# Kernel tuning notes

Measured on AMD Instinct MI355X. Metric: run time of the kernel, lower is better.

The kernel has to match this reference:

```python
import jax, jax.numpy as jnp
import numpy as np

N_E = 8192
E_DIM = 256
BETA = 0.25


def setup_inputs() -> dict:
    key = jax.random.key(0)
    kz, ke = jax.random.split(key)
    z = jax.random.normal(kz, (16, E_DIM, 32, 32), dtype=jnp.float32)
    embedding = jax.random.uniform(ke, (N_E, E_DIM), dtype=jnp.float32,
                                   minval=-1.0 / N_E, maxval=1.0 / N_E)
    return {"z": z, "embedding": embedding}


def reference(z, embedding):
    n_e, e_dim = embedding.shape
    # (B, C, H, W) -> (B, H, W, C) -> (N, e_dim)
    zp = jnp.transpose(z, (0, 2, 3, 1))
    zf = zp.reshape(-1, e_dim)
    # squared L2 distances: |z|^2 + |e|^2 - 2 z.e   -> (N, n_e)
    dists = (jnp.sum(zf * zf, axis=1, keepdims=True)
             + jnp.sum(embedding * embedding, axis=1)
             - 2.0 * (zf @ embedding.T))
    # two smallest distances (top-2 of negated dists)
    _, top2_idx = jax.lax.top_k(-dists, 2)
    min_encoding_indices = top2_idx[:, 0:1]
    second_encoding_indices = top2_idx[:, 1:2]
    min_encodings = jax.nn.one_hot(top2_idx[:, 0], n_e, dtype=zp.dtype)  # (N, n_e)
    z_q = (min_encodings @ embedding).reshape(zp.shape)
    # commitment / codebook loss
    loss = (jnp.mean((jax.lax.stop_gradient(z_q) - zp) ** 2)
            + BETA * jnp.mean((z_q - jax.lax.stop_gradient(zp)) ** 2))
    # straight-through estimator
    z_q = zp + jax.lax.stop_gradient(z_q - zp)
    avg_probs = jnp.mean(min_encodings, axis=0)
    perplexity = jnp.exp(-jnp.sum(avg_probs * jnp.log(avg_probs + 1e-10)))
    z_q = jnp.transpose(z_q, (0, 3, 1, 2))
    return (loss, z_q, perplexity, min_encodings,
            min_encoding_indices, second_encoding_indices)
```

## Files before the change

### kernel.cpp

```cpp
#include <hip/hip_runtime.h>
#include <cfloat>
#include <cstdint>
#include <cstddef>

#define M_ROWS 16384
#define NE     8192
#define KD     256

#define OFF_LOSS   0ULL
#define OFF_ZQ     1ULL
#define OFF_PERP   4194305ULL
#define OFF_ONEHOT 4194306ULL
#define OFF_I0     138412034ULL
#define OFF_I1     138428418ULL

#define SCR_Z16  0ULL
#define SCR_E16  2097152ULL
#define SCR_Z32T 3145728ULL
#define SCR_PART 7340032ULL

#define WS_I0    0
#define WS_HIST  16384
#define WS_ENORM 24576
#define WS_CNORM 32768
#define WS_T0SUM 49152
#define WS_TOTAL 49154

typedef _Float16 fp16x8 __attribute__((ext_vector_type(8)));
typedef float    floatx16 __attribute__((ext_vector_type(16)));

__global__ void zero_onehot_kernel(float* __restrict__ out) {
    size_t tidg = (size_t)blockIdx.x * 1024 + threadIdx.x;
    float4* base = (float4*)(out + OFF_ONEHOT + 2);
    const float4 zz = make_float4(0.f, 0.f, 0.f, 0.f);
#pragma unroll
    for (int i = 0; i < 8; i++) {
        size_t q = tidg + (size_t)i * 4194304ULL;
        if (q < 33554431ULL) base[q] = zz;
    }
    if (tidg == 0) {
        out[OFF_ONEHOT + 0] = 0.f;
        out[OFF_ONEHOT + 1] = 0.f;
        out[OFF_ONEHOT + 134217726ULL] = 0.f;
        out[OFF_ONEHOT + 134217727ULL] = 0.f;
    }
}

__global__ void scatter_ones_kernel(const int* __restrict__ ws_i0, float* __restrict__ out) {
    int r = blockIdx.x * 256 + threadIdx.x;
    int j = ws_i0[r] & (NE - 1);
    out[OFF_ONEHOT + (size_t)r * NE + j] = 1.0f;
}

__device__ __forceinline__ float pairwise16_sq(const float* row, int lane16) {
    const int h = lane16 >> 3, j = lane16 & 7;
    const float* p = row + h * 128 + j;
    float x = p[0];
    float r = __fmul_rn(x, x);
#pragma unroll
    for (int i = 1; i < 16; i++) {
        float y = p[i * 8];
        r = __fadd_rn(r, __fmul_rn(y, y));
    }
    float s = __fadd_rn(r, __shfl_xor(r, 1));
    s = __fadd_rn(s, __shfl_xor(s, 2));
    s = __fadd_rn(s, __shfl_xor(s, 4));
    s = __fadd_rn(s, __shfl_xor(s, 8));
    return s;
}

__global__ void split_e_kernel(const float* __restrict__ emb, _Float16* __restrict__ e16,
                               float* __restrict__ enorm, int* __restrict__ hist,
                               float* __restrict__ wsf) {
    __shared__ float ef[16][261];
    const int tid = threadIdx.x;
    const int row0 = blockIdx.x * 16;
#pragma unroll
    for (int p = 0; p < 4; p++) {
        int q = p * 256 + tid;
        int rl = q >> 6, kq = q & 63;
        float4 v = *(const float4*)(emb + (size_t)(row0 + rl) * KD + kq * 4);
        ef[rl][kq * 4 + 0] = v.x; ef[rl][kq * 4 + 1] = v.y;
        ef[rl][kq * 4 + 2] = v.z; ef[rl][kq * 4 + 3] = v.w;
    }
    __syncthreads();
#pragma unroll
    for (int p = 0; p < 2; p++) {
        int u = p * 256 + tid;
        int rl = u >> 5, k8g = u & 31;
        int code = row0 + rl;
        fp16x8 vh;
#pragma unroll
        for (int e = 0; e < 8; e++) vh[e] = (_Float16)(ef[rl][k8g * 8 + e] * 256.0f);
        int kb = k8g >> 2, k8 = k8g & 3;
        size_t unit = ((size_t)(code >> 7) * 8 + kb) * 512 + (size_t)(code & 127) * 4 + (k8 ^ (code & 3));
        *(fp16x8*)(e16 + unit * 8) = vh;
    }
    {
        int rl = tid >> 4, lane16 = tid & 15;
        float s = pairwise16_sq(&ef[rl][0], lane16);
        if (lane16 == 0) enorm[row0 + rl] = s;
    }
    if (blockIdx.x < 32) hist[blockIdx.x * 256 + tid] = 0;
    if (blockIdx.x == 32 && tid < 2) wsf[WS_T0SUM + tid] = 0.0f;
}

__global__ void split_z_kernel(const float* __restrict__ z, _Float16* __restrict__ z16,
                               float* __restrict__ z32t, float* __restrict__ cnorm) {
    __shared__ float zf[64][261];
    const int tid = threadIdx.x;
    const int r0  = blockIdx.x * 64;
    const int b   = r0 >> 10;
    const int hw0 = r0 & 1023;
    const float* zb = z + ((size_t)b << 18) + hw0;
#pragma unroll
    for (int p = 0; p < 16; p++) {
        int q = p * 256 + tid;
        int c = q >> 4, hq = q & 15;
        float4 v = *(const float4*)(zb + ((size_t)c << 10) + hq * 4);
        zf[hq * 4 + 0][c] = v.x; zf[hq * 4 + 1][c] = v.y;
        zf[hq * 4 + 2][c] = v.z; zf[hq * 4 + 3][c] = v.w;
    }
    __syncthreads();
#pragma unroll
    for (int rr = 0; rr < 4; rr++) {
        int row = rr * 16 + (tid >> 4);
        float s = pairwise16_sq(&zf[row][0], tid & 15);
        if ((tid & 15) == 0) cnorm[r0 + row] = s;
    }
#pragma unroll
    for (int p = 0; p < 8; p++) {
        int u = p * 256 + tid;
        int row = u >> 5, k8g = u & 31;
        int r = r0 + row;
        fp16x8 vh;
#pragma unroll
        for (int e = 0; e < 8; e++) vh[e] = (_Float16)zf[row][k8g * 8 + e];
        int kb = k8g >> 2, k8 = k8g & 3;
        size_t unit = ((size_t)(r >> 7) * 8 + kb) * 512 + (size_t)(r & 127) * 4 + (k8 ^ (r & 3));
        *(fp16x8*)(z16 + unit * 8) = vh;
    }
#pragma unroll
    for (int p = 0; p < 16; p++) {
        int q = p * 256 + tid;
        int row = q >> 6, co = (q & 63) * 4;
        float4 v = make_float4(zf[row][co], zf[row][co + 1], zf[row][co + 2], zf[row][co + 3]);
        *(float4*)(z32t + (size_t)(r0 + row) * 256 + co) = v;
    }
}

__device__ __forceinline__ fp16x8 frag_ld(const _Float16* lds, int rc, int ku) {
    int slot = rc * 4 + (ku ^ (rc & 3));
    return *(const fp16x8*)(lds + slot * 8);
}

#define MFMA(d, a, b) d = __builtin_amdgcn_mfma_f32_32x32x16_f16(a, b, d, 0, 0, 0)

__device__ __forceinline__ void ins2(float t, int i, float& t0, int& i0, float& t1, int& i1) {
    if (t < t0 || (t == t0 && i < i0)) { t1 = t0; i1 = i0; t0 = t; i0 = i; }
    else if (t < t1 || (t == t1 && i < i1)) { t1 = t; i1 = i; }
}

__launch_bounds__(256, 4)
__global__ void mfma_top2_kernel(const _Float16* __restrict__ e16, const _Float16* __restrict__ z16,
                                 const float* __restrict__ enorm_g, const float* __restrict__ cnorm_g,
                                 float4* __restrict__ part) {
    __shared__ _Float16 As[2][4096];
    __shared__ _Float16 Bs[2][4096];
    __shared__ float enb[128];
    __shared__ float mbuf[128][4];

    const int tid = threadIdx.x;
    const int lane = tid & 63, wid = tid >> 6;
    const int l31 = lane & 31, half = lane >> 5;
    const int wave_m = wid & 1, wave_n = wid >> 1;
    const int id = blockIdx.x;
    const int xcd = id & 7, slot = id >> 3;
    const int mtile = slot >> 4;
    const int ntile = (xcd << 4) | (slot & 15);

    const float4* Ap = (const float4*)(e16 + (size_t)mtile * 8 * 512 * 8);
    const float4* Bp = (const float4*)(z16 + (size_t)ntile * 8 * 512 * 8);

    if (tid < 128) enb[tid] = enorm_g[mtile * 128 + tid];
    float Cn[2];
    Cn[0] = cnorm_g[ntile * 128 + wave_n * 64 + l31];
    Cn[1] = cnorm_g[ntile * 128 + wave_n * 64 + 32 + l31];

    const int rcA0 = wave_m * 64 + l31, rcA1 = rcA0 + 32;
    const int rcB0 = wave_n * 64 + l31, rcB1 = rcB0 + 32;

    {
        float4 ra0 = Ap[tid], ra1 = Ap[256 + tid];
        float4 rb0 = Bp[tid], rb1 = Bp[256 + tid];
        ((float4*)As[0])[tid] = ra0; ((float4*)As[0])[256 + tid] = ra1;
        ((float4*)Bs[0])[tid] = rb0; ((float4*)Bs[0])[256 + tid] = rb1;
    }
    __syncthreads();

    floatx16 acc00 = (floatx16)0.f, acc01 = (floatx16)0.f,
             acc10 = (floatx16)0.f, acc11 = (floatx16)0.f;

    for (int kb = 0; kb < 8; kb++) {
        const int cur = kb & 1;
        float4 ra0, ra1, rb0, rb1;
        if (kb < 7) {
            const int nb = (kb + 1) * 512;
            ra0 = Ap[nb + tid]; ra1 = Ap[nb + 256 + tid];
            rb0 = Bp[nb + tid]; rb1 = Bp[nb + 256 + tid];
        }
#pragma unroll
        for (int ks = 0; ks < 2; ks++) {
            const int ku = ks * 2 + half;
            fp16x8 a0 = frag_ld(As[cur], rcA0, ku);
            fp16x8 a1 = frag_ld(As[cur], rcA1, ku);
            fp16x8 b0 = frag_ld(Bs[cur], rcB0, ku);
            fp16x8 b1 = frag_ld(Bs[cur], rcB1, ku);
            MFMA(acc00, a0, b0);
            MFMA(acc01, a0, b1);
            MFMA(acc10, a1, b0);
            MFMA(acc11, a1, b1);
        }
        if (kb < 7) {
            ((float4*)As[cur ^ 1])[tid] = ra0; ((float4*)As[cur ^ 1])[256 + tid] = ra1;
            ((float4*)Bs[cur ^ 1])[tid] = rb0; ((float4*)Bs[cur ^ 1])[256 + tid] = rb1;
        }
        __syncthreads();
    }

    float t0s[2] = {FLT_MAX, FLT_MAX}, t1s[2] = {FLT_MAX, FLT_MAX};
    int   i0s[2] = {0x7fffffff, 0x7fffffff}, i1s[2] = {0x7fffffff, 0x7fffffff};
#pragma unroll
    for (int mt = 0; mt < 2; mt++) {
#pragma unroll
        for (int reg = 0; reg < 16; reg++) {
            const int rl = (reg & 3) + 8 * (reg >> 2) + 4 * half;
            const int cloc = wave_m * 64 + mt * 32 + rl;
            const int code = mtile * 128 + cloc;
            const float E = enb[cloc];
            float g0 = (mt == 0) ? acc00[reg] : acc10[reg];
            float g1 = (mt == 0) ? acc01[reg] : acc11[reg];
            ins2(fmaf(-0.0078125f, g0, Cn[0] + E), code, t0s[0], i0s[0], t1s[0], i1s[0]);
            ins2(fmaf(-0.0078125f, g1, Cn[1] + E), code, t0s[1], i0s[1], t1s[1], i1s[1]);
        }
    }
#pragma unroll
    for (int s = 0; s < 2; s++) {
        float o0 = __shfl_xor(t0s[s], 32), o1 = __shfl_xor(t1s[s], 32);
        int  oi0 = __shfl_xor(i0s[s], 32), oi1 = __shfl_xor(i1s[s], 32);
        ins2(o0, oi0, t0s[s], i0s[s], t1s[s], i1s[s]);
        ins2(o1, oi1, t0s[s], i0s[s], t1s[s], i1s[s]);
    }
    __syncthreads();
    if (wave_m == 1 && lane < 32) {
#pragma unroll
        for (int s = 0; s < 2; s++) {
            int zr = wave_n * 64 + s * 32 + l31;
            mbuf[zr][0] = t0s[s]; mbuf[zr][1] = t1s[s];
            mbuf[zr][2] = __int_as_float(i0s[s]); mbuf[zr][3] = __int_as_float(i1s[s]);
        }
    }
    __syncthreads();
    if (wave_m == 0 && lane < 32) {
#pragma unroll
        for (int s = 0; s < 2; s++) {
            int zr = wave_n * 64 + s * 32 + l31;
            ins2(mbuf[zr][0], __float_as_int(mbuf[zr][2]), t0s[s], i0s[s], t1s[s], i1s[s]);
            ins2(mbuf[zr][1], __float_as_int(mbuf[zr][3]), t0s[s], i0s[s], t1s[s], i1s[s]);
            float4 o;
            o.x = t0s[s]; o.y = t1s[s];
            o.z = __int_as_float(i0s[s]); o.w = __int_as_float(i1s[s]);
            part[(size_t)(ntile * 128 + zr) * 64 + mtile] = o;
        }
    }
}

__global__ void rescore_kernel(const float* __restrict__ z32t, const float* __restrict__ emb,
                               const float* __restrict__ enorm_g, const float* __restrict__ cnorm_g,
                               const float4* __restrict__ part, float* __restrict__ out,
                               int* __restrict__ ws_i0, int* __restrict__ hist,
                               double* __restrict__ t0sum) {
    const int tid  = threadIdx.x;
    const int lane = tid & 63, wid = tid >> 6;
    const int r = blockIdx.x * 4 + wid;

    float4 p = part[(size_t)r * 64 + lane];
    const float tv0 = p.x, tv1 = p.y;
    const int jv0 = __float_as_int(p.z), jv1 = __float_as_int(p.w);

    float a = fminf(tv0, tv1), bmx = fmaxf(tv0, tv1);
#pragma unroll
    for (int m = 1; m < 64; m <<= 1) {
        float oa = __shfl_xor(a, m), ob = __shfl_xor(bmx, m);
        float na = fminf(a, oa);
        bmx = fminf(fmaxf(a, oa), fminf(bmx, ob));
        a = na;
    }
    const float T = bmx + 1.2e-4f;
    const float C = cnorm_g[r];

    const int c4 = lane * 4;
    float4 zv = *(const float4*)(z32t + (size_t)r * 256 + c4);
    const double zv0 = (double)zv.x, zv1 = (double)zv.y, zv2 = (double)zv.z, zv3 = (double)zv.w;

    float bt0 = FLT_MAX, bt1 = FLT_MAX;
    int   bi0 = NE - 1, bi1 = NE - 1;
    unsigned long long msk[2];
    msk[0] = __ballot(tv0 <= T);
    msk[1] = __ballot(tv1 <= T);
    for (int pass = 0; pass < 2; pass++) {
        unsigned long long mm = msk[pass];
        while (mm) {
            int g = __builtin_ctzll(mm);
            mm &= mm - 1;
            int j = __shfl(pass ? jv1 : jv0, g) & (NE - 1);
            float4 ev = *(const float4*)(emb + ((size_t)j << 8) + c4);
            double gl = zv0 * (double)ev.x + zv1 * (double)ev.y +
                        zv2 * (double)ev.z + zv3 * (double)ev.w;
#pragma unroll
            for (int m = 1; m < 64; m <<= 1) gl += __shfl_xor(gl, m);
            float g2 = (float)(2.0 * gl);
            float tex = (C + enorm_g[j]) - g2;
            if (tex < bt0 || (tex == bt0 && j < bi0)) {
                bt1 = bt0; bi1 = bi0; bt0 = tex; bi0 = j;
            } else if (tex < bt1 || (tex == bt1 && j < bi1)) {
                bt1 = tex; bi1 = j;
            }
        }
    }

    if (lane == 0) {
        out[OFF_I0 + r] = (float)bi0;
        out[OFF_I1 + r] = (float)bi1;
        ws_i0[r] = bi0;
        atomicAdd(&hist[bi0], 1);
    }
    __shared__ double red[4];
    if (lane == 0) red[wid] = (double)bt0;
    __syncthreads();
    if (tid == 0) atomicAdd(t0sum, (red[0] + red[1]) + (red[2] + red[3]));
}

__global__ void zq_kernel(const float* __restrict__ emb, const int* __restrict__ ws_i0,
                          float* __restrict__ out) {
    __shared__ float zt[64][65];
    const int tid = threadIdx.x;
    const int r0  = blockIdx.x * 64;
    const int b   = r0 >> 10;
    const int hw0 = r0 & 1023;
    const int kb  = blockIdx.y;
#pragma unroll
    for (int p = 0; p < 4; p++) {
        int q = p * 256 + tid;
        int row = q >> 4, co = (q & 15) * 4;
        int idx = ws_i0[r0 + row] & (NE - 1);
        float4 v = *(const float4*)(emb + ((size_t)idx << 8) + kb * 64 + co);
        zt[row][co + 0] = v.x; zt[row][co + 1] = v.y;
        zt[row][co + 2] = v.z; zt[row][co + 3] = v.w;
    }
    __syncthreads();
#pragma unroll
    for (int p = 0; p < 4; p++) {
        int q = p * 256 + tid;
        int c = q >> 4, h4 = (q & 15) * 4;
        float4 v = make_float4(zt[h4 + 0][c], zt[h4 + 1][c], zt[h4 + 2][c], zt[h4 + 3][c]);
        *(float4*)(out + OFF_ZQ + (((size_t)b * 256 + kb * 64 + c) << 10) + hw0 + h4) = v;
    }
}

__global__ void finalize_kernel(const int* __restrict__ hist, const double* __restrict__ t0sum,
                                float* __restrict__ out) {
    __shared__ float red[256];
    float s = 0.f;
    for (int j = threadIdx.x; j < NE; j += 256) {
        float p = (float)hist[j] * (1.0f / 16384.0f);
        s += p * logf(p + 1e-10f);
    }
    red[threadIdx.x] = s;
    __syncthreads();
    for (int m = 128; m; m >>= 1) {
        if (threadIdx.x < m) red[threadIdx.x] += red[threadIdx.x + m];
        __syncthreads();
    }
    if (threadIdx.x == 0) {
        out[OFF_PERP] = expf(-red[0]);
        out[OFF_LOSS] = 1.25f * (float)(t0sum[0] * (1.0 / 4194304.0));
    }
}

extern "C" void kernel_launch(void* const* d_in, const int* in_sizes, int n_in,
                              void* d_out, int out_size, void* d_ws, size_t ws_size,
                              hipStream_t stream) {
    const float* z   = (const float*)d_in[0];
    const float* emb = (const float*)d_in[1];
    float* out = (float*)d_out;
    float* ws  = (float*)d_ws;

    int*    ws_i0    = (int*)ws + WS_I0;
    int*    ws_hist  = (int*)ws + WS_HIST;
    float*  ws_enorm = ws + WS_ENORM;
    float*  ws_cnorm = ws + WS_CNORM;
    double* ws_t0sum = (double*)(ws + WS_T0SUM);

    float* scr = out + OFF_ONEHOT + 2;
    _Float16* z16 = (_Float16*)(scr + SCR_Z16);
    _Float16* e16 = (_Float16*)(scr + SCR_E16);
    float*  z32t  = scr + SCR_Z32T;
    float4* part  = (float4*)(scr + SCR_PART);

    hipLaunchKernelGGL(split_e_kernel, dim3(512), dim3(256), 0, stream,
                       emb, e16, ws_enorm, ws_hist, ws);
    hipLaunchKernelGGL(split_z_kernel, dim3(256), dim3(256), 0, stream,
                       z, z16, z32t, ws_cnorm);
    hipLaunchKernelGGL(mfma_top2_kernel, dim3(8192), dim3(256), 0, stream,
                       e16, z16, ws_enorm, ws_cnorm, part);
    hipLaunchKernelGGL(rescore_kernel, dim3(4096), dim3(256), 0, stream,
                       z32t, emb, ws_enorm, ws_cnorm, part, out, ws_i0, ws_hist, ws_t0sum);
    hipLaunchKernelGGL(zero_onehot_kernel, dim3(4096), dim3(1024), 0, stream, out);
    hipLaunchKernelGGL(scatter_ones_kernel, dim3(64), dim3(256), 0, stream, ws_i0, out);
    hipLaunchKernelGGL(zq_kernel, dim3(256, 4), dim3(256), 0, stream, emb, ws_i0, out);
    hipLaunchKernelGGL(finalize_kernel, dim3(1), dim3(256), 0, stream,
                       ws_hist, ws_t0sum, out);
}
```

Measured before the change: 1.074 ms.

## Keep a 256-row z tile resident in LDS and stream codebook tiles

The top-2 GEMM kernel is restructured so each 512-thread block loads 256 z rows (128KB fp16) into dynamic LDS once. It then streams 2048 codebook entries through a double-buffered LDS tile, with register prefetch four steps ahead. This cuts repeated global loads of z tiles across the many small 128x128 blocks. Partial top-2 results are now written per 128-code group, so the partial buffer doubles and the rescore kernel merges four candidates per lane instead of two. The cost is heavy LDS use that allows only one block per CU, a sync on every k-step, and possibly more rescore work.

Result: slower. 1.277 ms (+19.0%).

```diff
diff --git a/kernel.cpp b/kernel.cpp
--- a/kernel.cpp
+++ b/kernel.cpp
@@ -25,6 +25,8 @@
 #define WS_CNORM 32768
 #define WS_T0SUM 49152
 #define WS_TOTAL 49154
+
+#define SMEM_BYTES 155648
 
 typedef _Float16 fp16x8 __attribute__((ext_vector_type(8)));
 typedef float    floatx16 __attribute__((ext_vector_type(16)));
@@ -149,9 +151,14 @@
     }
 }
 
-__device__ __forceinline__ fp16x8 frag_ld(const _Float16* lds, int rc, int ku) {
+__device__ __forceinline__ fp16x8 efrag_ld(const _Float16* lds, int rc, int ku) {
     int slot = rc * 4 + (ku ^ (rc & 3));
     return *(const fp16x8*)(lds + slot * 8);
+}
+__device__ __forceinline__ fp16x8 zfrag_ld(const _Float16* Zs, int kb, int rloc, int ku) {
+    int sec = (rloc >> 7) * 8 + kb;
+    int slot = sec * 512 + (rloc & 127) * 4 + (ku ^ (rloc & 3));
+    return *(const fp16x8*)(Zs + slot * 8);
 }
 
 #define MFMA(d, a, b) d = __builtin_amdgcn_mfma_f32_32x32x16_f16(a, b, d, 0, 0, 0)
@@ -161,116 +168,102 @@
     else if (t < t1 || (t == t1 && i < i1)) { t1 = t; i1 = i; }
 }
 
-__launch_bounds__(256, 4)
+__launch_bounds__(512, 2)
 __global__ void mfma_top2_kernel(const _Float16* __restrict__ e16, const _Float16* __restrict__ z16,
                                  const float* __restrict__ enorm_g, const float* __restrict__ cnorm_g,
                                  float4* __restrict__ part) {
-    __shared__ _Float16 As[2][4096];
-    __shared__ _Float16 Bs[2][4096];
-    __shared__ float enb[128];
-    __shared__ float mbuf[128][4];
+    extern __shared__ char smem[];
+    _Float16* Zs  = (_Float16*)smem;
+    _Float16* Es0 = (_Float16*)(smem + 131072);
+    _Float16* Es1 = (_Float16*)(smem + 139264);
+    float*    enb = (float*)(smem + 147456);
 
     const int tid = threadIdx.x;
     const int lane = tid & 63, wid = tid >> 6;
     const int l31 = lane & 31, half = lane >> 5;
     const int wave_m = wid & 1, wave_n = wid >> 1;
-    const int id = blockIdx.x;
-    const int xcd = id & 7, slot = id >> 3;
-    const int mtile = slot >> 4;
-    const int ntile = (xcd << 4) | (slot & 15);
-
-    const float4* Ap = (const float4*)(e16 + (size_t)mtile * 8 * 512 * 8);
-    const float4* Bp = (const float4*)(z16 + (size_t)ntile * 8 * 512 * 8);
-
-    if (tid < 128) enb[tid] = enorm_g[mtile * 128 + tid];
+    const int cg = blockIdx.x;
+    const int nt = blockIdx.y;
+    const int r0 = nt * 256;
+
+    const float4* Zg = (const float4*)(z16 + (size_t)nt * 8192 * 8);
+    float4* Zl = (float4*)Zs;
+#pragma unroll
+    for (int p = 0; p < 16; p++) Zl[p * 512 + tid] = Zg[p * 512 + tid];
+#pragma unroll
+    for (int p = 0; p < 4; p++) enb[p * 512 + tid] = enorm_g[cg * 2048 + p * 512 + tid];
+
     float Cn[2];
-    Cn[0] = cnorm_g[ntile * 128 + wave_n * 64 + l31];
-    Cn[1] = cnorm_g[ntile * 128 + wave_n * 64 + 32 + l31];
+    Cn[0] = cnorm_g[r0 + wave_n * 64 + l31];
+    Cn[1] = cnorm_g[r0 + wave_n * 64 + 32 + l31];
 
     const int rcA0 = wave_m * 64 + l31, rcA1 = rcA0 + 32;
     const int rcB0 = wave_n * 64 + l31, rcB1 = rcB0 + 32;
 
-    {
-        float4 ra0 = Ap[tid], ra1 = Ap[256 + tid];
-        float4 rb0 = Bp[tid], rb1 = Bp[256 + tid];
-        ((float4*)As[0])[tid] = ra0; ((float4*)As[0])[256 + tid] = ra1;
-        ((float4*)Bs[0])[tid] = rb0; ((float4*)Bs[0])[256 + tid] = rb1;
-    }
-    __syncthreads();
-
-    floatx16 acc00 = (floatx16)0.f, acc01 = (floatx16)0.f,
-             acc10 = (floatx16)0.f, acc11 = (floatx16)0.f;
-
-    for (int kb = 0; kb < 8; kb++) {
-        const int cur = kb & 1;
-        float4 ra0, ra1, rb0, rb1;
-        if (kb < 7) {
-            const int nb = (kb + 1) * 512;
-            ra0 = Ap[nb + tid]; ra1 = Ap[nb + 256 + tid];
-            rb0 = Bp[nb + tid]; rb1 = Bp[nb + 256 + tid];
+    const float4* Eg = (const float4*)(e16 + (size_t)cg * 65536 * 8);
+    float4 q[4];
+#pragma unroll
+    for (int d = 0; d < 4; d++) q[d] = Eg[(size_t)d * 512 + tid];
+    ((float4*)Es0)[tid] = q[0];
+    __syncthreads();
+
+    for (int jt = 0; jt < 16; jt++) {
+        floatx16 acc00 = (floatx16)0.f, acc01 = (floatx16)0.f,
+                 acc10 = (floatx16)0.f, acc11 = (floatx16)0.f;
+#pragma unroll
+        for (int kb = 0; kb < 8; kb++) {
+            const int it = jt * 8 + kb;
+            if (it + 4 < 128) q[kb & 3] = Eg[(size_t)(it + 4) * 512 + tid];
+            if (it < 127) {
+                float4* dst = (float4*)((it & 1) ? Es0 : Es1);
+                dst[tid] = q[(kb + 1) & 3];
+            }
+            const _Float16* Ecur = (it & 1) ? Es1 : Es0;
+#pragma unroll
+            for (int ks = 0; ks < 2; ks++) {
+                const int ku = ks * 2 + half;
+                fp16x8 a0 = efrag_ld(Ecur, rcA0, ku);
+                fp16x8 a1 = efrag_ld(Ecur, rcA1, ku);
+                fp16x8 b0 = zfrag_ld(Zs, kb, rcB0, ku);
+                fp16x8 b1 = zfrag_ld(Zs, kb, rcB1, ku);
+                MFMA(acc00, a0, b0); MFMA(acc01, a0, b1);
+                MFMA(acc10, a1, b0); MFMA(acc11, a1, b1);
+            }
+            __syncthreads();
         }
-#pragma unroll
-        for (int ks = 0; ks < 2; ks++) {
-            const int ku = ks * 2 + half;
-            fp16x8 a0 = frag_ld(As[cur], rcA0, ku);
-            fp16x8 a1 = frag_ld(As[cur], rcA1, ku);
-            fp16x8 b0 = frag_ld(Bs[cur], rcB0, ku);
-            fp16x8 b1 = frag_ld(Bs[cur], rcB1, ku);
-            MFMA(acc00, a0, b0);
-            MFMA(acc01, a0, b1);
-            MFMA(acc10, a1, b0);
-            MFMA(acc11, a1, b1);
+        float t0s[2] = {FLT_MAX, FLT_MAX}, t1s[2] = {FLT_MAX, FLT_MAX};
+        int   i0s[2] = {0x7fffffff, 0x7fffffff}, i1s[2] = {0x7fffffff, 0x7fffffff};
+#pragma unroll
+        for (int mt = 0; mt < 2; mt++) {
+#pragma unroll
+            for (int reg = 0; reg < 16; reg++) {
+                const int rl = (reg & 3) + 8 * (reg >> 2) + 4 * half;
+                const int cloc = wave_m * 64 + mt * 32 + rl;
+                const int code = cg * 2048 + jt * 128 + cloc;
+                const float E = enb[jt * 128 + cloc];
+                float g0 = (mt == 0) ? acc00[reg] : acc10[reg];
+                float g1 = (mt == 0) ? acc01[reg] : acc11[reg];
+                ins2(fmaf(-0.0078125f, g0, Cn[0] + E), code, t0s[0], i0s[0], t1s[0], i1s[0]);
+                ins2(fmaf(-0.0078125f, g1, Cn[1] + E), code, t0s[1], i0s[1], t1s[1], i1s[1]);
+            }
         }
-        if (kb < 7) {
-            ((float4*)As[cur ^ 1])[tid] = ra0; ((float4*)As[cur ^ 1])[256 + tid] = ra1;
-            ((float4*)Bs[cur ^ 1])[tid] = rb0; ((float4*)Bs[cur ^ 1])[256 + tid] = rb1;
+#pragma unroll
+        for (int s = 0; s < 2; s++) {
+            float o0 = __shfl_xor(t0s[s], 32), o1 = __shfl_xor(t1s[s], 32);
+            int  oi0 = __shfl_xor(i0s[s], 32), oi1 = __shfl_xor(i1s[s], 32);
+            ins2(o0, oi0, t0s[s], i0s[s], t1s[s], i1s[s]);
+            ins2(o1, oi1, t0s[s], i0s[s], t1s[s], i1s[s]);
         }
-        __syncthreads();
-    }
-
-    float t0s[2] = {FLT_MAX, FLT_MAX}, t1s[2] = {FLT_MAX, FLT_MAX};
-    int   i0s[2] = {0x7fffffff, 0x7fffffff}, i1s[2] = {0x7fffffff, 0x7fffffff};
-#pragma unroll
-    for (int mt = 0; mt < 2; mt++) {
-#pragma unroll
-        for (int reg = 0; reg < 16; reg++) {
-            const int rl = (reg & 3) + 8 * (reg >> 2) + 4 * half;
-            const int cloc = wave_m * 64 + mt * 32 + rl;
-            const int code = mtile * 128 + cloc;
-            const float E = enb[cloc];
-            float g0 = (mt == 0) ? acc00[reg] : acc10[reg];
-            float g1 = (mt == 0) ? acc01[reg] : acc11[reg];
-            ins2(fmaf(-0.0078125f, g0, Cn[0] + E), code, t0s[0], i0s[0], t1s[0], i1s[0]);
-            ins2(fmaf(-0.0078125f, g1, Cn[1] + E), code, t0s[1], i0s[1], t1s[1], i1s[1]);
-        }
-    }
-#pragma unroll
-    for (int s = 0; s < 2; s++) {
-        float o0 = __shfl_xor(t0s[s], 32), o1 = __shfl_xor(t1s[s], 32);
-        int  oi0 = __shfl_xor(i0s[s], 32), oi1 = __shfl_xor(i1s[s], 32);
-        ins2(o0, oi0, t0s[s], i0s[s], t1s[s], i1s[s]);
-        ins2(o1, oi1, t0s[s], i0s[s], t1s[s], i1s[s]);
-    }
-    __syncthreads();
-    if (wave_m == 1 && lane < 32) {
-#pragma unroll
-        for (int s = 0; s < 2; s++) {
-            int zr = wave_n * 64 + s * 32 + l31;
-            mbuf[zr][0] = t0s[s]; mbuf[zr][1] = t1s[s];
-            mbuf[zr][2] = __int_as_float(i0s[s]); mbuf[zr][3] = __int_as_float(i1s[s]);
-        }
-    }
-    __syncthreads();
-    if (wave_m == 0 && lane < 32) {
-#pragma unroll
-        for (int s = 0; s < 2; s++) {
-            int zr = wave_n * 64 + s * 32 + l31;
-            ins2(mbuf[zr][0], __float_as_int(mbuf[zr][2]), t0s[s], i0s[s], t1s[s], i1s[s]);
-            ins2(mbuf[zr][1], __float_as_int(mbuf[zr][3]), t0s[s], i0s[s], t1s[s], i1s[s]);
-            float4 o;
-            o.x = t0s[s]; o.y = t1s[s];
-            o.z = __int_as_float(i0s[s]); o.w = __int_as_float(i1s[s]);
-            part[(size_t)(ntile * 128 + zr) * 64 + mtile] = o;
+        if (lane < 32) {
+            const int grp = cg * 32 + jt * 2 + wave_m;
+#pragma unroll
+            for (int s = 0; s < 2; s++) {
+                int zr = wave_n * 64 + s * 32 + l31;
+                float4 o;
+                o.x = t0s[s]; o.y = t1s[s];
+                o.z = __int_as_float(i0s[s]); o.w = __int_as_float(i1s[s]);
+                part[(size_t)(r0 + zr) * 128 + grp] = o;
+            }
         }
     }
 }
@@ -284,11 +277,16 @@
     const int lane = tid & 63, wid = tid >> 6;
     const int r = blockIdx.x * 4 + wid;
 
-    float4 p = part[(size_t)r * 64 + lane];
-    const float tv0 = p.x, tv1 = p.y;
-    const int jv0 = __float_as_int(p.z), jv1 = __float_as_int(p.w);
-
-    float a = fminf(tv0, tv1), bmx = fmaxf(tv0, tv1);
+    float4 pa = part[(size_t)r * 128 + lane];
+    float4 pb = part[(size_t)r * 128 + 64 + lane];
+    float v0 = pa.x, v1 = pa.y, v2 = pb.x, v3 = pb.y;
+    int   j0 = __float_as_int(pa.z), j1 = __float_as_int(pa.w);
+    int   j2 = __float_as_int(pb.z), j3 = __float_as_int(pb.w);
+
+    float m1 = fminf(v0, v1), M1 = fmaxf(v0, v1);
+    float n1 = fminf(v2, v3), N1 = fmaxf(v2, v3);
+    float a = fminf(m1, n1);
+    float bmx = fminf(fmaxf(m1, n1), fminf(M1, N1));
 #pragma unroll
     for (int m = 1; m < 64; m <<= 1) {
         float oa = __shfl_xor(a, m), ob = __shfl_xor(bmx, m);
@@ -305,15 +303,18 @@
 
     float bt0 = FLT_MAX, bt1 = FLT_MAX;
     int   bi0 = NE - 1, bi1 = NE - 1;
-    unsigned long long msk[2];
-    msk[0] = __ballot(tv0 <= T);
-    msk[1] = __ballot(tv1 <= T);
-    for (int pass = 0; pass < 2; pass++) {
+    unsigned long long msk[4];
+    msk[0] = __ballot(v0 <= T);
+    msk[1] = __ballot(v1 <= T);
+    msk[2] = __ballot(v2 <= T);
+    msk[3] = __ballot(v3 <= T);
+    const int jsel[4] = {j0, j1, j2, j3};
+    for (int pass = 0; pass < 4; pass++) {
         unsigned long long mm = msk[pass];
         while (mm) {
             int g = __builtin_ctzll(mm);
             mm &= mm - 1;
-            int j = __shfl(pass ? jv1 : jv0, g) & (NE - 1);
+            int j = __shfl(jsel[pass], g) & (NE - 1);
             float4 ev = *(const float4*)(emb + ((size_t)j << 8) + c4);
             double gl = zv0 * (double)ev.x + zv1 * (double)ev.y +
                         zv2 * (double)ev.z + zv3 * (double)ev.w;
@@ -408,11 +409,18 @@
     float*  z32t  = scr + SCR_Z32T;
     float4* part  = (float4*)(scr + SCR_PART);
 
+    static bool attr_set = false;
+    if (!attr_set) {
+        hipFuncSetAttribute((const void*)mfma_top2_kernel,
+                            hipFuncAttributeMaxDynamicSharedMemorySize, SMEM_BYTES);
+        attr_set = true;
+    }
+
     hipLaunchKernelGGL(split_e_kernel, dim3(512), dim3(256), 0, stream,
                        emb, e16, ws_enorm, ws_hist, ws);
     hipLaunchKernelGGL(split_z_kernel, dim3(256), dim3(256), 0, stream,
                        z, z16, z32t, ws_cnorm);
-    hipLaunchKernelGGL(mfma_top2_kernel, dim3(8192), dim3(256), 0, stream,
+    hipLaunchKernelGGL(mfma_top2_kernel, dim3(4, 64), dim3(512), SMEM_BYTES, stream,
                        e16, z16, ws_enorm, ws_cnorm, part);
     hipLaunchKernelGGL(rescore_kernel, dim3(4096), dim3(256), 0, stream,
                        z32t, emb, ws_enorm, ws_cnorm, part, out, ws_i0, ws_hist, ws_t0sum);
```

## Switch distance GEMM to FP8 MFMA with per-tile top-4 candidates and wider rescore

Applied to the files above, without the earlier changes.

Quantizes z and the codebook to FP8 e4m3, with the codebook scaled by 32768, and runs the distance GEMM with the fp8 32x32x16 MFMA. This halves the operand bytes and raises matrix throughput. To make up for the coarser precision, each tile keeps its top-4 candidates instead of top-2, and the rescore pass loosens its threshold so that more candidates get exact fp64 rescoring. The grid becomes 2D, which drops the XCD-aware tile remapping. The costs are more rescore work, more partial-buffer traffic, and a risk of missing the true nearest code if FP8 error exceeds the margin.

Measured after the change: 1.553 ms. +44.6%, slower.

```diff
diff --git a/kernel.cpp b/kernel.cpp
--- a/kernel.cpp
+++ b/kernel.cpp
@@ -1,4 +1,5 @@
 #include <hip/hip_runtime.h>
+#include <hip/hip_fp8.h>
 #include <cfloat>
 #include <cstdint>
 #include <cstddef>
@@ -14,10 +15,10 @@
 #define OFF_I0     138412034ULL
 #define OFF_I1     138428418ULL
 
-#define SCR_Z16  0ULL
-#define SCR_E16  2097152ULL
-#define SCR_Z32T 3145728ULL
-#define SCR_PART 7340032ULL
+#define SCR_Z8   0ULL
+#define SCR_E8   1048576ULL
+#define SCR_Z32T 1572864ULL
+#define SCR_PART 5767168ULL
 
 #define WS_I0    0
 #define WS_HIST  16384
@@ -26,8 +27,12 @@
 #define WS_T0SUM 49152
 #define WS_TOTAL 49154
 
-typedef _Float16 fp16x8 __attribute__((ext_vector_type(8)));
-typedef float    floatx16 __attribute__((ext_vector_type(16)));
+typedef float floatx16 __attribute__((ext_vector_type(16)));
+
+__device__ __forceinline__ unsigned char to_fp8(float x) {
+    __hip_fp8_e4m3 h(x);
+    return h.__x;
+}
 
 __global__ void zero_onehot_kernel(float* __restrict__ out) {
     size_t tidg = (size_t)blockIdx.x * 1024 + threadIdx.x;
@@ -69,7 +74,7 @@
     return s;
 }
 
-__global__ void split_e_kernel(const float* __restrict__ emb, _Float16* __restrict__ e16,
+__global__ void split_e_kernel(const float* __restrict__ emb, unsigned char* __restrict__ e8,
                                float* __restrict__ enorm, int* __restrict__ hist,
                                float* __restrict__ wsf) {
     __shared__ float ef[16][261];
@@ -89,12 +94,13 @@
         int u = p * 256 + tid;
         int rl = u >> 5, k8g = u & 31;
         int code = row0 + rl;
-        fp16x8 vh;
-#pragma unroll
-        for (int e = 0; e < 8; e++) vh[e] = (_Float16)(ef[rl][k8g * 8 + e] * 256.0f);
+        unsigned long long pk = 0;
+#pragma unroll
+        for (int e = 0; e < 8; e++)
+            pk |= (unsigned long long)to_fp8(ef[rl][k8g * 8 + e] * 32768.0f) << (8 * e);
         int kb = k8g >> 2, k8 = k8g & 3;
         size_t unit = ((size_t)(code >> 7) * 8 + kb) * 512 + (size_t)(code & 127) * 4 + (k8 ^ (code & 3));
-        *(fp16x8*)(e16 + unit * 8) = vh;
+        *(unsigned long long*)(e8 + unit * 8) = pk;
     }
     {
         int rl = tid >> 4, lane16 = tid & 15;
@@ -105,7 +111,7 @@
     if (blockIdx.x == 32 && tid < 2) wsf[WS_T0SUM + tid] = 0.0f;
 }
 
-__global__ void split_z_kernel(const float* __restrict__ z, _Float16* __restrict__ z16,
+__global__ void split_z_kernel(const float* __restrict__ z, unsigned char* __restrict__ z8,
                                float* __restrict__ z32t, float* __restrict__ cnorm) {
     __shared__ float zf[64][261];
     const int tid = threadIdx.x;
@@ -133,12 +139,13 @@
         int u = p * 256 + tid;
         int row = u >> 5, k8g = u & 31;
         int r = r0 + row;
-        fp16x8 vh;
-#pragma unroll
-        for (int e = 0; e < 8; e++) vh[e] = (_Float16)zf[row][k8g * 8 + e];
+        unsigned long long pk = 0;
+#pragma unroll
+        for (int e = 0; e < 8; e++)
+            pk |= (unsigned long long)to_fp8(zf[row][k8g * 8 + e]) << (8 * e);
         int kb = k8g >> 2, k8 = k8g & 3;
         size_t unit = ((size_t)(r >> 7) * 8 + kb) * 512 + (size_t)(r & 127) * 4 + (k8 ^ (r & 3));
-        *(fp16x8*)(z16 + unit * 8) = vh;
+        *(unsigned long long*)(z8 + unit * 8) = pk;
     }
 #pragma unroll
     for (int p = 0; p < 16; p++) {
@@ -149,38 +156,49 @@
     }
 }
 
-__device__ __forceinline__ fp16x8 frag_ld(const _Float16* lds, int rc, int ku) {
+__device__ __forceinline__ long long frag8(const unsigned char* lds, int rc, int ku) {
     int slot = rc * 4 + (ku ^ (rc & 3));
-    return *(const fp16x8*)(lds + slot * 8);
-}
-
-#define MFMA(d, a, b) d = __builtin_amdgcn_mfma_f32_32x32x16_f16(a, b, d, 0, 0, 0)
-
-__device__ __forceinline__ void ins2(float t, int i, float& t0, int& i0, float& t1, int& i1) {
-    if (t < t0 || (t == t0 && i < i0)) { t1 = t0; i1 = i0; t0 = t; i0 = i; }
-    else if (t < t1 || (t == t1 && i < i1)) { t1 = t; i1 = i; }
+    return *(const long long*)(lds + slot * 8);
+}
+
+#define MFMA8(d, a, b) d = __builtin_amdgcn_mfma_f32_32x32x16_fp8_fp8(a, b, d, 0, 0, 0)
+
+__device__ __forceinline__ bool lex_lt(float t, int i, float T, int I) {
+    return (t < T) || (t == T && i < I);
+}
+__device__ __forceinline__ void ins4(float t, int i,
+    float& t0, int& i0, float& t1, int& i1,
+    float& t2, int& i2, float& t3, int& i3) {
+    if (lex_lt(t, i, t3, i3)) {
+        if (lex_lt(t, i, t2, i2)) {
+            t3 = t2; i3 = i2;
+            if (lex_lt(t, i, t1, i1)) {
+                t2 = t1; i2 = i1;
+                if (lex_lt(t, i, t0, i0)) { t1 = t0; i1 = i0; t0 = t; i0 = i; }
+                else { t1 = t; i1 = i; }
+            } else { t2 = t; i2 = i; }
+        } else { t3 = t; i3 = i; }
+    }
 }
 
 __launch_bounds__(256, 4)
-__global__ void mfma_top2_kernel(const _Float16* __restrict__ e16, const _Float16* __restrict__ z16,
+__global__ void mfma_top4_kernel(const unsigned char* __restrict__ e8, const unsigned char* __restrict__ z8,
                                  const float* __restrict__ enorm_g, const float* __restrict__ cnorm_g,
                                  float4* __restrict__ part) {
-    __shared__ _Float16 As[2][4096];
-    __shared__ _Float16 Bs[2][4096];
+    __shared__ unsigned char As[2][4096];
+    __shared__ unsigned char Bs[2][4096];
     __shared__ float enb[128];
-    __shared__ float mbuf[128][4];
+    __shared__ float mbuf[128][8];
 
     const int tid = threadIdx.x;
     const int lane = tid & 63, wid = tid >> 6;
     const int l31 = lane & 31, half = lane >> 5;
     const int wave_m = wid & 1, wave_n = wid >> 1;
-    const int id = blockIdx.x;
-    const int xcd = id & 7, slot = id >> 3;
-    const int mtile = slot >> 4;
-    const int ntile = (xcd << 4) | (slot & 15);
-
-    const float4* Ap = (const float4*)(e16 + (size_t)mtile * 8 * 512 * 8);
-    const float4* Bp = (const float4*)(z16 + (size_t)ntile * 8 * 512 * 8);
+    const int mtile = blockIdx.x;
+    const int ntile = blockIdx.y;
+
+    const float4* Ap = (const float4*)(e8 + (size_t)mtile * 32768);
+    const float4* Bp = (const float4*)(z8 + (size_t)ntile * 32768);
 
     if (tid < 128) enb[tid] = enorm_g[mtile * 128 + tid];
     float Cn[2];
@@ -191,10 +209,9 @@
     const int rcB0 = wave_n * 64 + l31, rcB1 = rcB0 + 32;
 
     {
-        float4 ra0 = Ap[tid], ra1 = Ap[256 + tid];
-        float4 rb0 = Bp[tid], rb1 = Bp[256 + tid];
-        ((float4*)As[0])[tid] = ra0; ((float4*)As[0])[256 + tid] = ra1;
-        ((float4*)Bs[0])[tid] = rb0; ((float4*)Bs[0])[256 + tid] = rb1;
+        float4 ra = Ap[tid], rb = Bp[tid];
+        ((float4*)As[0])[tid] = ra;
+        ((float4*)Bs[0])[tid] = rb;
     }
     __syncthreads();
 
@@ -203,33 +220,37 @@
 
     for (int kb = 0; kb < 8; kb++) {
         const int cur = kb & 1;
-        float4 ra0, ra1, rb0, rb1;
+        float4 ra, rb;
         if (kb < 7) {
-            const int nb = (kb + 1) * 512;
-            ra0 = Ap[nb + tid]; ra1 = Ap[nb + 256 + tid];
-            rb0 = Bp[nb + tid]; rb1 = Bp[nb + 256 + tid];
+            ra = Ap[(kb + 1) * 256 + tid];
+            rb = Bp[(kb + 1) * 256 + tid];
         }
 #pragma unroll
         for (int ks = 0; ks < 2; ks++) {
             const int ku = ks * 2 + half;
-            fp16x8 a0 = frag_ld(As[cur], rcA0, ku);
-            fp16x8 a1 = frag_ld(As[cur], rcA1, ku);
-            fp16x8 b0 = frag_ld(Bs[cur], rcB0, ku);
-            fp16x8 b1 = frag_ld(Bs[cur], rcB1, ku);
-            MFMA(acc00, a0, b0);
-            MFMA(acc01, a0, b1);
-            MFMA(acc10, a1, b0);
-            MFMA(acc11, a1, b1);
+            long long a0 = frag8(As[cur], rcA0, ku);
+            long long a1 = frag8(As[cur], rcA1, ku);
+            long long b0 = frag8(Bs[cur], rcB0, ku);
+            long long b1 = frag8(Bs[cur], rcB1, ku);
+            MFMA8(acc00, a0, b0);
+            MFMA8(acc01, a0, b1);
+            MFMA8(acc10, a1, b0);
+            MFMA8(acc11, a1, b1);
         }
         if (kb < 7) {
-            ((float4*)As[cur ^ 1])[tid] = ra0; ((float4*)As[cur ^ 1])[256 + tid] = ra1;
-            ((float4*)Bs[cur ^ 1])[tid] = rb0; ((float4*)Bs[cur ^ 1])[256 + tid] = rb1;
+            ((float4*)As[cur ^ 1])[tid] = ra;
+            ((float4*)Bs[cur ^ 1])[tid] = rb;
         }
         __syncthreads();
     }
 
-    float t0s[2] = {FLT_MAX, FLT_MAX}, t1s[2] = {FLT_MAX, FLT_MAX};
-    int   i0s[2] = {0x7fffffff, 0x7fffffff}, i1s[2] = {0x7fffffff, 0x7fffffff};
+    float q0[2], q1[2], q2[2], q3[2];
+    int   j0[2], j1[2], j2[2], j3[2];
+#pragma unroll
+    for (int s = 0; s < 2; s++) {
+        q0[s] = q1[s] = q2[s] = q3[s] = FLT_MAX;
+        j0[s] = j1[s] = j2[s] = j3[s] = 0x7fffffff;
+    }
 #pragma unroll
     for (int mt = 0; mt < 2; mt++) {
 #pragma unroll
@@ -240,24 +261,31 @@
             const float E = enb[cloc];
             float g0 = (mt == 0) ? acc00[reg] : acc10[reg];
             float g1 = (mt == 0) ? acc01[reg] : acc11[reg];
-            ins2(fmaf(-0.0078125f, g0, Cn[0] + E), code, t0s[0], i0s[0], t1s[0], i1s[0]);
-            ins2(fmaf(-0.0078125f, g1, Cn[1] + E), code, t0s[1], i0s[1], t1s[1], i1s[1]);
+            float ta = fmaf(-6.103515625e-05f, g0, Cn[0] + E);
+            ins4(ta, code, q0[0], j0[0], q1[0], j1[0], q2[0], j2[0], q3[0], j3[0]);
+            float tb = fmaf(-6.103515625e-05f, g1, Cn[1] + E);
+            ins4(tb, code, q0[1], j0[1], q1[1], j1[1], q2[1], j2[1], q3[1], j3[1]);
         }
     }
 #pragma unroll
     for (int s = 0; s < 2; s++) {
-        float o0 = __shfl_xor(t0s[s], 32), o1 = __shfl_xor(t1s[s], 32);
-        int  oi0 = __shfl_xor(i0s[s], 32), oi1 = __shfl_xor(i1s[s], 32);
-        ins2(o0, oi0, t0s[s], i0s[s], t1s[s], i1s[s]);
-        ins2(o1, oi1, t0s[s], i0s[s], t1s[s], i1s[s]);
+        float o0 = __shfl_xor(q0[s], 32), o1 = __shfl_xor(q1[s], 32),
+              o2 = __shfl_xor(q2[s], 32), o3 = __shfl_xor(q3[s], 32);
+        int  p0 = __shfl_xor(j0[s], 32), p1 = __shfl_xor(j1[s], 32),
+             p2 = __shfl_xor(j2[s], 32), p3 = __shfl_xor(j3[s], 32);
+        ins4(o0, p0, q0[s], j0[s], q1[s], j1[s], q2[s], j2[s], q3[s], j3[s]);
+        ins4(o1, p1, q0[s], j0[s], q1[s], j1[s], q2[s], j2[s], q3[s], j3[s]);
+        ins4(o2, p2, q0[s], j0[s], q1[s], j1[s], q2[s], j2[s], q3[s], j3[s]);
+        ins4(o3, p3, q0[s], j0[s], q1[s], j1[s], q2[s], j2[s], q3[s], j3[s]);
     }
     __syncthreads();
     if (wave_m == 1 && lane < 32) {
 #pragma unroll
         for (int s = 0; s < 2; s++) {
             int zr = wave_n * 64 + s * 32 + l31;
-            mbuf[zr][0] = t0s[s]; mbuf[zr][1] = t1s[s];
-            mbuf[zr][2] = __int_as_float(i0s[s]); mbuf[zr][3] = __int_as_float(i1s[s]);
+            mbuf[zr][0] = q0[s]; mbuf[zr][1] = q1[s]; mbuf[zr][2] = q2[s]; mbuf[zr][3] = q3[s];
+            mbuf[zr][4] = __int_as_float(j0[s]); mbuf[zr][5] = __int_as_float(j1[s]);
+            mbuf[zr][6] = __int_as_float(j2[s]); mbuf[zr][7] = __int_as_float(j3[s]);
         }
     }
     __syncthreads();
@@ -265,12 +293,22 @@
 #pragma unroll
         for (int s = 0; s < 2; s++) {
             int zr = wave_n * 64 + s * 32 + l31;
-            ins2(mbuf[zr][0], __float_as_int(mbuf[zr][2]), t0s[s], i0s[s], t1s[s], i1s[s]);
-            ins2(mbuf[zr][1], __float_as_int(mbuf[zr][3]), t0s[s], i0s[s], t1s[s], i1s[s]);
-            float4 o;
-            o.x = t0s[s]; o.y = t1s[s];
-            o.z = __int_as_float(i0s[s]); o.w = __int_as_float(i1s[s]);
-            part[(size_t)(ntile * 128 + zr) * 64 + mtile] = o;
+            ins4(mbuf[zr][0], __float_as_int(mbuf[zr][4]),
+                 q0[s], j0[s], q1[s], j1[s], q2[s], j2[s], q3[s], j3[s]);
+            ins4(mbuf[zr][1], __float_as_int(mbuf[zr][5]),
+                 q0[s], j0[s], q1[s], j1[s], q2[s], j2[s], q3[s], j3[s]);
+            ins4(mbuf[zr][2], __float_as_int(mbuf[zr][6]),
+                 q0[s], j0[s], q1[s], j1[s], q2[s], j2[s], q3[s], j3[s]);
+            ins4(mbuf[zr][3], __float_as_int(mbuf[zr][7]),
+                 q0[s], j0[s], q1[s], j1[s], q2[s], j2[s], q3[s], j3[s]);
+            size_t base = ((size_t)(ntile * 128 + zr) * 64 + mtile) * 2;
+            float4 oa, ob;
+            oa.x = q0[s]; oa.y = q1[s];
+            oa.z = __int_as_float(j0[s]); oa.w = __int_as_float(j1[s]);
+            ob.x = q2[s]; ob.y = q3[s];
+            ob.z = __int_as_float(j2[s]); ob.w = __int_as_float(j3[s]);
+            part[base] = oa;
+            part[base + 1] = ob;
         }
     }
 }
@@ -284,11 +322,16 @@
     const int lane = tid & 63, wid = tid >> 6;
     const int r = blockIdx.x * 4 + wid;
 
-    float4 p = part[(size_t)r * 64 + lane];
-    const float tv0 = p.x, tv1 = p.y;
-    const int jv0 = __float_as_int(p.z), jv1 = __float_as_int(p.w);
-
-    float a = fminf(tv0, tv1), bmx = fmaxf(tv0, tv1);
+    float4 pa = part[(size_t)r * 128 + lane];
+    float4 pb = part[(size_t)r * 128 + 64 + lane];
+    float v0 = pa.x, v1 = pa.y, v2 = pb.x, v3 = pb.y;
+    int   j0 = __float_as_int(pa.z), j1 = __float_as_int(pa.w);
+    int   j2 = __float_as_int(pb.z), j3 = __float_as_int(pb.w);
+
+    float m1 = fminf(v0, v1), M1 = fmaxf(v0, v1);
+    float n1 = fminf(v2, v3), N1 = fmaxf(v2, v3);
+    float a = fminf(m1, n1);
+    float bmx = fminf(fmaxf(m1, n1), fminf(M1, N1));
 #pragma unroll
     for (int m = 1; m < 64; m <<= 1) {
         float oa = __shfl_xor(a, m), ob = __shfl_xor(bmx, m);
@@ -296,7 +339,7 @@
         bmx = fminf(fmaxf(a, oa), fminf(bmx, ob));
         a = na;
     }
-    const float T = bmx + 1.2e-4f;
+    const float T = bmx + 1.5e-3f;
     const float C = cnorm_g[r];
 
     const int c4 = lane * 4;
@@ -305,15 +348,18 @@
 
     float bt0 = FLT_MAX, bt1 = FLT_MAX;
     int   bi0 = NE - 1, bi1 = NE - 1;
-    unsigned long long msk[2];
-    msk[0] = __ballot(tv0 <= T);
-    msk[1] = __ballot(tv1 <= T);
-    for (int pass = 0; pass < 2; pass++) {
+    unsigned long long msk[4];
+    msk[0] = __ballot(v0 <= T);
+    msk[1] = __ballot(v1 <= T);
+    msk[2] = __ballot(v2 <= T);
+    msk[3] = __ballot(v3 <= T);
+    const int jsel[4] = {j0, j1, j2, j3};
+    for (int pass = 0; pass < 4; pass++) {
         unsigned long long mm = msk[pass];
         while (mm) {
             int g = __builtin_ctzll(mm);
             mm &= mm - 1;
-            int j = __shfl(pass ? jv1 : jv0, g) & (NE - 1);
+            int j = __shfl(jsel[pass], g) & (NE - 1);
             float4 ev = *(const float4*)(emb + ((size_t)j << 8) + c4);
             double gl = zv0 * (double)ev.x + zv1 * (double)ev.y +
                         zv2 * (double)ev.z + zv3 * (double)ev.w;
@@ -403,17 +449,17 @@
     double* ws_t0sum = (double*)(ws + WS_T0SUM);
 
     float* scr = out + OFF_ONEHOT + 2;
-    _Float16* z16 = (_Float16*)(scr + SCR_Z16);
-    _Float16* e16 = (_Float16*)(scr + SCR_E16);
+    unsigned char* z8 = (unsigned char*)(scr + SCR_Z8);
+    unsigned char* e8 = (unsigned char*)(scr + SCR_E8);
     float*  z32t  = scr + SCR_Z32T;
     float4* part  = (float4*)(scr + SCR_PART);
 
     hipLaunchKernelGGL(split_e_kernel, dim3(512), dim3(256), 0, stream,
-                       emb, e16, ws_enorm, ws_hist, ws);
+                       emb, e8, ws_enorm, ws_hist, ws);
     hipLaunchKernelGGL(split_z_kernel, dim3(256), dim3(256), 0, stream,
-                       z, z16, z32t, ws_cnorm);
-    hipLaunchKernelGGL(mfma_top2_kernel, dim3(8192), dim3(256), 0, stream,
-                       e16, z16, ws_enorm, ws_cnorm, part);
+                       z, z8, z32t, ws_cnorm);
+    hipLaunchKernelGGL(mfma_top4_kernel, dim3(64, 128), dim3(256), 0, stream,
+                       e8, z8, ws_enorm, ws_cnorm, part);
     hipLaunchKernelGGL(rescore_kernel, dim3(4096), dim3(256), 0, stream,
                        z32t, emb, ws_enorm, ws_cnorm, part, out, ws_i0, ws_hist, ws_t0sum);
     hipLaunchKernelGGL(zero_onehot_kernel, dim3(4096), dim3(1024), 0, stream, out);
```
